# Optimization experiments

Measured on AMD Instinct MI355X. Metric: run time of the kernel, lower is better.

## Reference

```python
import jax, jax.numpy as jnp
import numpy as np

HEADS = 8
DIM_HEAD = 64
SCALE = DIM_HEAD ** -0.5


def setup_inputs() -> dict:
    key = jax.random.key(0)
    k1, k2, k3, k4 = jax.random.split(key, 4)
    b, c, f, h, w = 2, 512, 16, 32, 32
    x = jax.random.normal(k1, (b, c, f, h, w), dtype=jnp.float32)
    pos_bias = jax.random.normal(k2, (HEADS, f, f), dtype=jnp.float32)
    # torch Linear(dim, 3*hidden, bias=False): store as (in, out) for right-matmul
    w_qkv = jax.random.normal(k3, (c, 3 * HEADS * DIM_HEAD), dtype=jnp.float32) * (c ** -0.5)
    w_out = jax.random.normal(k4, (HEADS * DIM_HEAD, c), dtype=jnp.float32) * ((HEADS * DIM_HEAD) ** -0.5)
    return {"x": x, "pos_bias": pos_bias, "w_qkv": w_qkv, "w_out": w_out}


def reference(x, pos_bias, w_qkv, w_out):
    b, c, f, h, w = x.shape
    # 'b c f h w -> (b h w) f c'
    xt = jnp.transpose(x, (0, 3, 4, 2, 1)).reshape(b * h * w, f, c)
    qkv = xt @ w_qkv  # (B, f, 3*hidden)
    q, k, v = jnp.split(qkv, 3, axis=-1)
    def to_heads(t):  # (B, f, h*d) -> (B, heads, f, d)
        return t.reshape(t.shape[0], f, HEADS, DIM_HEAD).transpose(0, 2, 1, 3)
    q, k, v = to_heads(q) * SCALE, to_heads(k), to_heads(v)
    sim = jnp.einsum('bhid,bhjd->bhij', q, k)
    sim = sim + pos_bias  # (heads, f, f) broadcasts over batch
    attn = jax.nn.softmax(sim, axis=-1)  # stable max-subtract softmax
    out = jnp.einsum('bhij,bhjd->bhid', attn, v)
    out = out.transpose(0, 2, 1, 3).reshape(b * h * w, f, HEADS * DIM_HEAD)
    out = out @ w_out  # (B, f, c)
    # '(b h w) f c -> b c f h w'
    return out.reshape(b, h, w, f, c).transpose(0, 4, 3, 1, 2)
```

## Files before the change

kernel.cpp:

```cpp
#include <hip/hip_runtime.h>

typedef unsigned short u16;
typedef unsigned int u32;
typedef unsigned long long u64;
typedef __attribute__((ext_vector_type(8))) short short8;
typedef __attribute__((ext_vector_type(4))) float f32x4;

__device__ __forceinline__ u16 f2bf(float f) {
  u32 u = __builtin_bit_cast(u32, f);
  u += 0x7fffu + ((u >> 16) & 1u);
  return (u16)(u >> 16);
}
__device__ __forceinline__ u32 pk2bf(float a, float b) {
  return (u32)f2bf(a) | ((u32)f2bf(b) << 16);
}

__device__ __forceinline__ void async16(const void* g, void* l) {
  __builtin_amdgcn_global_load_lds(
      (const __attribute__((address_space(1))) u32*)g,
      (__attribute__((address_space(3))) u32*)l, 16, 0, 0);
}

__global__ __launch_bounds__(256) void k_wt(const float* __restrict__ in,
                                            u16* __restrict__ outT,
                                            int K, int N, int scaleN, int perm) {
  const int bid = blockIdx.x;
  const int ntiles = N >> 5;
  const int nt = bid % ntiles, kt = bid / ntiles;
  const int n0 = nt << 5, k0 = kt << 5;
  __shared__ float tile[32][33];
  const int t = threadIdx.x;
#pragma unroll
  for (int i = 0; i < 4; ++i) {
    const int e = t + i * 256, r = e >> 5, c = e & 31;
    tile[c][r] = in[(size_t)(k0 + r) * N + n0 + c];
  }
  __syncthreads();
#pragma unroll
  for (int i = 0; i < 4; ++i) {
    const int e = t + i * 256, r = e >> 5, c = e & 31;
    float v = tile[r][c];
    if (n0 + r < scaleN) v *= 0.125f;
    const int kcol = k0 + c;
    const int kp = perm ? ((kcol & ~63) | ((kcol & 15) << 2) | ((kcol >> 4) & 3))
                        : kcol;
    outT[(size_t)(n0 + r) * K + kp] = f2bf(v);
  }
}

__global__ __launch_bounds__(256) void k_xt(const float* __restrict__ x,
                                            u16* __restrict__ XT) {
  const int bid = blockIdx.x;
  const int plane = bid & 31;
  const int rest = bid >> 5;
  const int mt = rest & 31, ct = rest >> 5;
  const int bb = plane >> 4, f = plane & 15;
  const int m0 = mt << 5, c0 = ct << 5;
  __shared__ float tile[32][36];
  const int t = threadIdx.x;
  const int lr = t >> 3, lc = t & 7;
  const float4 v4 = *(const float4*)
      &x[((size_t)((bb * 512 + c0 + lr) * 16 + f)) * 1024 + m0 + lc * 4];
  *(float4*)&tile[lr][lc * 4] = v4;
  __syncthreads();
  const int m = t >> 3, cc = t & 7;
  union { u32 uu[2]; u64 q; } pk;
  pk.uu[0] = pk2bf(tile[cc * 4 + 0][m], tile[cc * 4 + 1][m]);
  pk.uu[1] = pk2bf(tile[cc * 4 + 2][m], tile[cc * 4 + 3][m]);
  *(u64*)&XT[((size_t)((bb * 1024 + m0 + m) * 16 + f)) * 512 + c0 + cc * 4] = pk.q;
}

struct A3St { u16 A[128][64]; u16 B[192][64]; };
struct A3At { u16 q[8][16][64]; u16 k[8][16][64]; u16 vt[8][64][16]; u16 pad[16]; };
union A3Sm { A3St st; A3At at; };

__global__ __launch_bounds__(256) void k_qkv_attn(const u16* __restrict__ XT,
                                                  const u16* __restrict__ WQ,
                                                  const float* __restrict__ pos_bias,
                                                  u16* __restrict__ AO) {
  const int tid = threadIdx.x;
  const int w = tid >> 6, lane = tid & 63;
  const int c15 = lane & 15, quad = lane >> 4;
  const int bid = blockIdx.x;
  const int hd = bid >> 8, m0 = (bid & 255) << 7;

  __shared__ A3Sm sm;

  const int lr = lane >> 3, lcb = lane & 7;

  const u16* aptr[4];
  const u16* bptr[6];
#pragma unroll
  for (int t2 = 0; t2 < 4; ++t2) {
    const int r = w * 32 + t2 * 8 + lr;
    aptr[t2] = XT + (size_t)(m0 + r) * 512 + ((lcb ^ (r & 7)) << 3);
  }
#pragma unroll
  for (int t2 = 0; t2 < 6; ++t2) {
    const int j = w * 48 + t2 * 8 + lr;
    const int grow = (j >> 6) * 512 + hd * 64 + (j & 63);
    bptr[t2] = WQ + (size_t)grow * 512 + ((lcb ^ (j & 7)) << 3);
  }

  f32x4 acc[3][8];
#pragma unroll
  for (int c = 0; c < 3; ++c)
#pragma unroll
    for (int mt = 0; mt < 8; ++mt) acc[c][mt] = f32x4{0.f, 0.f, 0.f, 0.f};

#pragma unroll
  for (int kk = 0; kk < 8; ++kk) {
    __syncthreads();
#pragma unroll
    for (int t2 = 0; t2 < 4; ++t2)
      async16(aptr[t2] + (kk << 6), &sm.st.A[w * 32 + t2 * 8][0]);
#pragma unroll
    for (int t2 = 0; t2 < 6; ++t2)
      async16(bptr[t2] + (kk << 6), &sm.st.B[w * 48 + t2 * 8][0]);
    __syncthreads();
#pragma unroll
    for (int half = 0; half < 2; ++half) {
      short8 af[8], bt[3];
#pragma unroll
      for (int mt = 0; mt < 8; ++mt) {
        const int row = mt * 16 + c15;
        const int swz = (((half << 2) + quad) ^ (row & 7)) << 3;
        af[mt] = *(const short8*)&sm.st.A[row][swz];
      }
#pragma unroll
      for (int c = 0; c < 3; ++c) {
        const int row = c * 64 + w * 16 + c15;
        const int swz = (((half << 2) + quad) ^ (row & 7)) << 3;
        bt[c] = *(const short8*)&sm.st.B[row][swz];
      }
#pragma unroll
      for (int c = 0; c < 3; ++c)
#pragma unroll
        for (int mt = 0; mt < 8; ++mt)
          acc[c][mt] = __builtin_amdgcn_mfma_f32_16x16x32_bf16(af[mt], bt[c], acc[c][mt], 0, 0, 0);
    }
  }
  __syncthreads();

  const int dloc = w * 16 + c15;
  const int ch_b = dloc >> 3, dl = dloc & 7;
#pragma unroll
  for (int mt = 0; mt < 8; ++mt) {
#pragma unroll
    for (int r = 0; r < 4; ++r) {
      const int f = quad * 4 + r;
      const int sw = ((ch_b ^ (f & 7)) << 3) | dl;
      sm.at.q[mt][f][sw] = f2bf(acc[0][mt][r]);
      sm.at.k[mt][f][sw] = f2bf(acc[1][mt][r]);
    }
    union { u32 uu[2]; u64 q; } pv;
    pv.uu[0] = pk2bf(acc[2][mt][0], acc[2][mt][1]);
    pv.uu[1] = pk2bf(acc[2][mt][2], acc[2][mt][3]);
    *(u64*)&sm.at.vt[mt][dloc][quad * 4] = pv.q;
  }
  __syncthreads();

  float pb[4];
#pragma unroll
  for (int r = 0; r < 4; ++r)
    pb[r] = pos_bias[hd * 256 + (quad * 4 + r) * 16 + c15];

  for (int sblk = 0; sblk < 2; ++sblk) {
    const int s = w * 2 + sblk;
    f32x4 sacc = f32x4{0.f, 0.f, 0.f, 0.f};
#pragma unroll
    for (int h = 0; h < 2; ++h) {
      const int chunk = (((h << 2) + quad) ^ (c15 & 7)) << 3;
      const short8 aq = *(const short8*)&sm.at.q[s][c15][chunk];
      const short8 bk = *(const short8*)&sm.at.k[s][c15][chunk];
      sacc = __builtin_amdgcn_mfma_f32_16x16x32_bf16(aq, bk, sacc, 0, 0, 0);
    }
    asm volatile("" ::: "memory");
    u16* lp = &sm.at.q[s][0][0];
#pragma unroll
    for (int e = 0; e < 4; ++e) lp[c15 * 32 + 16 + quad * 4 + e] = 0;
#pragma unroll
    for (int r = 0; r < 4; ++r) {
      float sv = sacc[r] + pb[r];
      float mx = sv;
      mx = fmaxf(mx, __shfl_xor(mx, 1));
      mx = fmaxf(mx, __shfl_xor(mx, 2));
      mx = fmaxf(mx, __shfl_xor(mx, 4));
      mx = fmaxf(mx, __shfl_xor(mx, 8));
      const float e = __expf(sv - mx);
      float sum = e;
      sum += __shfl_xor(sum, 1);
      sum += __shfl_xor(sum, 2);
      sum += __shfl_xor(sum, 4);
      sum += __shfl_xor(sum, 8);
      lp[(quad * 4 + r) * 32 + c15] = f2bf(e / sum);
    }
    asm volatile("" ::: "memory");
    const short8 ap = *(const short8*)&lp[c15 * 32 + quad * 8];
    f32x4 oacc[4];
#pragma unroll
    for (int t = 0; t < 4; ++t) {
      const short8 bv = *(const short8*)&sm.at.vt[s][t * 16 + c15][(quad & 1) * 8];
      oacc[t] = __builtin_amdgcn_mfma_f32_16x16x32_bf16(ap, bv, f32x4{0.f, 0.f, 0.f, 0.f}, 0, 0, 0);
    }
    const int s_g = (m0 >> 4) + s;
    const int bb = s_g >> 10, sp = s_g & 1023;
#pragma unroll
    for (int r = 0; r < 4; ++r) {
      union { u32 uu[2]; uint2 v; } pk;
      pk.uu[0] = pk2bf(oacc[0][r], oacc[1][r]);
      pk.uu[1] = pk2bf(oacc[2][r], oacc[3][r]);
      *(uint2*)(AO + ((size_t)(bb * 16384 + (quad * 4 + r) * 1024 + sp)) * 512 +
                hd * 64 + c15 * 4) = pk.v;
    }
  }
}

struct K2St { u16 A[128][64]; u16 B[128][64]; };
union K2Sm { K2St st; float C[64][130]; };

__global__ __launch_bounds__(256) void k_proj(const u16* __restrict__ AO,
                                              const u16* __restrict__ WO,
                                              float* __restrict__ out) {
  const int tid = threadIdx.x, w = tid >> 6, lane = tid & 63;
  const int c15 = lane & 15, quad = lane >> 4;
  const int bid = blockIdx.x;
  const int mb = bid & 255, nb = bid >> 8;
  const int m0 = mb << 7, n0 = nb << 7;
  const int b = m0 >> 14, mloc = m0 & 16383;
  __shared__ K2Sm sm;
  f32x4 acc[8][2];
#pragma unroll
  for (int mt = 0; mt < 8; ++mt) {
    acc[mt][0] = f32x4{0.f, 0.f, 0.f, 0.f};
    acc[mt][1] = f32x4{0.f, 0.f, 0.f, 0.f};
  }
  const int lr = lane >> 3, lcb = lane & 7;
  const u16* aptr[4];
  const u16* bptr[4];
#pragma unroll
  for (int t2 = 0; t2 < 4; ++t2) {
    const int r = w * 32 + t2 * 8 + lr;
    const int sw = (lcb ^ (r & 7)) << 3;
    aptr[t2] = AO + (size_t)(m0 + r) * 512 + sw;
    bptr[t2] = WO + (size_t)(n0 + r) * 512 + sw;
  }
#pragma unroll
  for (int kk = 0; kk < 8; ++kk) {
    __syncthreads();
#pragma unroll
    for (int t2 = 0; t2 < 4; ++t2) {
      async16(aptr[t2] + (kk << 6), &sm.st.A[w * 32 + t2 * 8][0]);
      async16(bptr[t2] + (kk << 6), &sm.st.B[w * 32 + t2 * 8][0]);
    }
    __syncthreads();
#pragma unroll
    for (int half = 0; half < 2; ++half) {
      short8 af[8], bt[2];
#pragma unroll
      for (int mt = 0; mt < 8; ++mt) {
        const int row = mt * 16 + c15;
        const int swz = (((half << 2) + quad) ^ (row & 7)) << 3;
        af[mt] = *(const short8*)&sm.st.A[row][swz];
      }
#pragma unroll
      for (int nt = 0; nt < 2; ++nt) {
        const int row = w * 32 + nt * 16 + c15;
        const int swz = (((half << 2) + quad) ^ (row & 7)) << 3;
        bt[nt] = *(const short8*)&sm.st.B[row][swz];
      }
#pragma unroll
      for (int mt = 0; mt < 8; ++mt) {
        acc[mt][0] = __builtin_amdgcn_mfma_f32_16x16x32_bf16(af[mt], bt[0], acc[mt][0], 0, 0, 0);
        acc[mt][1] = __builtin_amdgcn_mfma_f32_16x16x32_bf16(af[mt], bt[1], acc[mt][1], 0, 0, 0);
      }
    }
  }
  __syncthreads();
#pragma unroll
  for (int h = 0; h < 2; ++h) {
#pragma unroll
    for (int mt2 = 0; mt2 < 4; ++mt2) {
      const int mt = h * 4 + mt2;
#pragma unroll
      for (int nt = 0; nt < 2; ++nt)
#pragma unroll
        for (int r = 0; r < 4; ++r)
          sm.C[mt2 * 16 + quad * 4 + r][w * 32 + nt * 16 + c15] = acc[mt][nt][r];
    }
    __syncthreads();
    for (int jj = 0; jj < 32; ++jj) {
      const int ch = n0 + w * 32 + jj;
      out[(size_t)(b * 512 + ch) * 16384 + mloc + h * 64 + lane] = sm.C[lane][w * 32 + jj];
    }
    __syncthreads();
  }
}

extern "C" void kernel_launch(void* const* d_in, const int* in_sizes, int n_in,
                              void* d_out, int out_size, void* d_ws, size_t ws_size,
                              hipStream_t stream) {
  const float* x = (const float*)d_in[0];
  const float* pos_bias = (const float*)d_in[1];
  const float* w_qkv = (const float*)d_in[2];
  const float* w_out = (const float*)d_in[3];
  float* out = (float*)d_out;
  char* ws = (char*)d_ws;
  u16* XT = (u16*)(ws);
  u16* AO = (u16*)(ws + (size_t)33554432);
  u16* WQ = (u16*)(ws + (size_t)67108864);
  u16* WO = (u16*)(ws + (size_t)68681728);

  hipLaunchKernelGGL(k_wt, dim3(768), dim3(256), 0, stream, w_qkv, WQ, 512, 1536, 512, 0);
  hipLaunchKernelGGL(k_wt, dim3(256), dim3(256), 0, stream, w_out, WO, 512, 512, 0, 1);
  hipLaunchKernelGGL(k_xt, dim3(16384), dim3(256), 0, stream, x, XT);
  hipLaunchKernelGGL(k_qkv_attn, dim3(2048), dim3(256), 0, stream, XT, WQ, pos_bias, AO);
  hipLaunchKernelGGL(k_proj, dim3(1024), dim3(256), 0, stream, AO, WO, out);
}
```

Measured before the change: 242.4 us.

## Double-buffer K-loop LDS tiles with async prefetch in QKV and projection GEMMs

Both GEMM kernels now split each K step into 32-wide chunks held in two LDS buffers. The global-to-LDS async load of the next chunk is issued before the MFMAs on the current chunk, with one barrier per iteration instead of two. This is meant to hide global load latency behind matrix math. In exchange there are twice as many loop iterations, a narrower 4-way swizzle that may add LDS bank conflicts, and a reliance on the trailing barrier to order the async loads.

After: 244.8 us. About the same (+1.0%).

```diff
diff --git a/kernel.cpp b/kernel.cpp
--- a/kernel.cpp
+++ b/kernel.cpp
@@ -70,9 +70,9 @@
   *(u64*)&XT[((size_t)((bb * 1024 + m0 + m) * 16 + f)) * 512 + c0 + cc * 4] = pk.q;
 }
 
-struct A3St { u16 A[128][64]; u16 B[192][64]; };
+struct A3St32 { u16 A[128][32]; u16 B[192][32]; };
 struct A3At { u16 q[8][16][64]; u16 k[8][16][64]; u16 vt[8][64][16]; u16 pad[16]; };
-union A3Sm { A3St st; A3At at; };
+union A3Sm { A3St32 st[2]; A3At at; };
 
 __global__ __launch_bounds__(256) void k_qkv_attn(const u16* __restrict__ XT,
                                                   const u16* __restrict__ WQ,
@@ -86,20 +86,20 @@
 
   __shared__ A3Sm sm;
 
-  const int lr = lane >> 3, lcb = lane & 7;
-
-  const u16* aptr[4];
-  const u16* bptr[6];
-#pragma unroll
-  for (int t2 = 0; t2 < 4; ++t2) {
-    const int r = w * 32 + t2 * 8 + lr;
-    aptr[t2] = XT + (size_t)(m0 + r) * 512 + ((lcb ^ (r & 7)) << 3);
-  }
-#pragma unroll
-  for (int t2 = 0; t2 < 6; ++t2) {
-    const int j = w * 48 + t2 * 8 + lr;
+  const int lr16 = lane >> 2, lc4 = lane & 3;
+
+  const u16* aptr[2];
+  const u16* bptr[3];
+#pragma unroll
+  for (int t2 = 0; t2 < 2; ++t2) {
+    const int r = w * 32 + t2 * 16 + lr16;
+    aptr[t2] = XT + (size_t)(m0 + r) * 512 + ((lc4 ^ (r & 3)) << 3);
+  }
+#pragma unroll
+  for (int t2 = 0; t2 < 3; ++t2) {
+    const int j = w * 48 + t2 * 16 + lr16;
     const int grow = (j >> 6) * 512 + hd * 64 + (j & 63);
-    bptr[t2] = WQ + (size_t)grow * 512 + ((lcb ^ (j & 7)) << 3);
+    bptr[t2] = WQ + (size_t)grow * 512 + ((lc4 ^ (j & 3)) << 3);
   }
 
   f32x4 acc[3][8];
@@ -109,38 +109,44 @@
     for (int mt = 0; mt < 8; ++mt) acc[c][mt] = f32x4{0.f, 0.f, 0.f, 0.f};
 
 #pragma unroll
-  for (int kk = 0; kk < 8; ++kk) {
+  for (int t2 = 0; t2 < 2; ++t2)
+    async16(aptr[t2], &sm.st[0].A[w * 32 + t2 * 16][0]);
+#pragma unroll
+  for (int t2 = 0; t2 < 3; ++t2)
+    async16(bptr[t2], &sm.st[0].B[w * 48 + t2 * 16][0]);
+  __syncthreads();
+
+#pragma unroll
+  for (int kk = 0; kk < 16; ++kk) {
+    const int cur = kk & 1, nxt = cur ^ 1;
+    if (kk < 15) {
+#pragma unroll
+      for (int t2 = 0; t2 < 2; ++t2)
+        async16(aptr[t2] + ((kk + 1) << 5), &sm.st[nxt].A[w * 32 + t2 * 16][0]);
+#pragma unroll
+      for (int t2 = 0; t2 < 3; ++t2)
+        async16(bptr[t2] + ((kk + 1) << 5), &sm.st[nxt].B[w * 48 + t2 * 16][0]);
+    }
+    short8 af[8], bt[3];
+#pragma unroll
+    for (int mt = 0; mt < 8; ++mt) {
+      const int row = mt * 16 + c15;
+      const int swz = (quad ^ (row & 3)) << 3;
+      af[mt] = *(const short8*)&sm.st[cur].A[row][swz];
+    }
+#pragma unroll
+    for (int c = 0; c < 3; ++c) {
+      const int row = c * 64 + w * 16 + c15;
+      const int swz = (quad ^ (row & 3)) << 3;
+      bt[c] = *(const short8*)&sm.st[cur].B[row][swz];
+    }
+#pragma unroll
+    for (int c = 0; c < 3; ++c)
+#pragma unroll
+      for (int mt = 0; mt < 8; ++mt)
+        acc[c][mt] = __builtin_amdgcn_mfma_f32_16x16x32_bf16(af[mt], bt[c], acc[c][mt], 0, 0, 0);
     __syncthreads();
-#pragma unroll
-    for (int t2 = 0; t2 < 4; ++t2)
-      async16(aptr[t2] + (kk << 6), &sm.st.A[w * 32 + t2 * 8][0]);
-#pragma unroll
-    for (int t2 = 0; t2 < 6; ++t2)
-      async16(bptr[t2] + (kk << 6), &sm.st.B[w * 48 + t2 * 8][0]);
-    __syncthreads();
-#pragma unroll
-    for (int half = 0; half < 2; ++half) {
-      short8 af[8], bt[3];
-#pragma unroll
-      for (int mt = 0; mt < 8; ++mt) {
-        const int row = mt * 16 + c15;
-        const int swz = (((half << 2) + quad) ^ (row & 7)) << 3;
-        af[mt] = *(const short8*)&sm.st.A[row][swz];
-      }
-#pragma unroll
-      for (int c = 0; c < 3; ++c) {
-        const int row = c * 64 + w * 16 + c15;
-        const int swz = (((half << 2) + quad) ^ (row & 7)) << 3;
-        bt[c] = *(const short8*)&sm.st.B[row][swz];
-      }
-#pragma unroll
-      for (int c = 0; c < 3; ++c)
-#pragma unroll
-        for (int mt = 0; mt < 8; ++mt)
-          acc[c][mt] = __builtin_amdgcn_mfma_f32_16x16x32_bf16(af[mt], bt[c], acc[c][mt], 0, 0, 0);
-    }
-  }
-  __syncthreads();
+  }
 
   const int dloc = w * 16 + c15;
   const int ch_b = dloc >> 3, dl = dloc & 7;
@@ -216,8 +222,8 @@
   }
 }
 
-struct K2St { u16 A[128][64]; u16 B[128][64]; };
-union K2Sm { K2St st; float C[64][130]; };
+struct K2St32 { u16 A[128][32]; u16 B[128][32]; };
+union K2Sm { K2St32 st[2]; float C[64][130]; };
 
 __global__ __launch_bounds__(256) void k_proj(const u16* __restrict__ AO,
                                               const u16* __restrict__ WO,
@@ -235,48 +241,53 @@
     acc[mt][0] = f32x4{0.f, 0.f, 0.f, 0.f};
     acc[mt][1] = f32x4{0.f, 0.f, 0.f, 0.f};
   }
-  const int lr = lane >> 3, lcb = lane & 7;
-  const u16* aptr[4];
-  const u16* bptr[4];
-#pragma unroll
-  for (int t2 = 0; t2 < 4; ++t2) {
-    const int r = w * 32 + t2 * 8 + lr;
-    const int sw = (lcb ^ (r & 7)) << 3;
+  const int lr16 = lane >> 2, lc4 = lane & 3;
+  const u16* aptr[2];
+  const u16* bptr[2];
+#pragma unroll
+  for (int t2 = 0; t2 < 2; ++t2) {
+    const int r = w * 32 + t2 * 16 + lr16;
+    const int sw = (lc4 ^ (r & 3)) << 3;
     aptr[t2] = AO + (size_t)(m0 + r) * 512 + sw;
     bptr[t2] = WO + (size_t)(n0 + r) * 512 + sw;
   }
 #pragma unroll
-  for (int kk = 0; kk < 8; ++kk) {
+  for (int t2 = 0; t2 < 2; ++t2) {
+    async16(aptr[t2], &sm.st[0].A[w * 32 + t2 * 16][0]);
+    async16(bptr[t2], &sm.st[0].B[w * 32 + t2 * 16][0]);
+  }
+  __syncthreads();
+
+#pragma unroll
+  for (int kk = 0; kk < 16; ++kk) {
+    const int cur = kk & 1, nxt = cur ^ 1;
+    if (kk < 15) {
+#pragma unroll
+      for (int t2 = 0; t2 < 2; ++t2) {
+        async16(aptr[t2] + ((kk + 1) << 5), &sm.st[nxt].A[w * 32 + t2 * 16][0]);
+        async16(bptr[t2] + ((kk + 1) << 5), &sm.st[nxt].B[w * 32 + t2 * 16][0]);
+      }
+    }
+    short8 af[8], bt[2];
+#pragma unroll
+    for (int mt = 0; mt < 8; ++mt) {
+      const int row = mt * 16 + c15;
+      const int swz = (quad ^ (row & 3)) << 3;
+      af[mt] = *(const short8*)&sm.st[cur].A[row][swz];
+    }
+#pragma unroll
+    for (int nt = 0; nt < 2; ++nt) {
+      const int row = w * 32 + nt * 16 + c15;
+      const int swz = (quad ^ (row & 3)) << 3;
+      bt[nt] = *(const short8*)&sm.st[cur].B[row][swz];
+    }
+#pragma unroll
+    for (int mt = 0; mt < 8; ++mt) {
+      acc[mt][0] = __builtin_amdgcn_mfma_f32_16x16x32_bf16(af[mt], bt[0], acc[mt][0], 0, 0, 0);
+      acc[mt][1] = __builtin_amdgcn_mfma_f32_16x16x32_bf16(af[mt], bt[1], acc[mt][1], 0, 0, 0);
+    }
     __syncthreads();
-#pragma unroll
-    for (int t2 = 0; t2 < 4; ++t2) {
-      async16(aptr[t2] + (kk << 6), &sm.st.A[w * 32 + t2 * 8][0]);
-      async16(bptr[t2] + (kk << 6), &sm.st.B[w * 32 + t2 * 8][0]);
-    }
-    __syncthreads();
-#pragma unroll
-    for (int half = 0; half < 2; ++half) {
-      short8 af[8], bt[2];
-#pragma unroll
-      for (int mt = 0; mt < 8; ++mt) {
-        const int row = mt * 16 + c15;
-        const int swz = (((half << 2) + quad) ^ (row & 7)) << 3;
-        af[mt] = *(const short8*)&sm.st.A[row][swz];
-      }
-#pragma unroll
-      for (int nt = 0; nt < 2; ++nt) {
-        const int row = w * 32 + nt * 16 + c15;
-        const int swz = (((half << 2) + quad) ^ (row & 7)) << 3;
-        bt[nt] = *(const short8*)&sm.st.B[row][swz];
-      }
-#pragma unroll
-      for (int mt = 0; mt < 8; ++mt) {
-        acc[mt][0] = __builtin_amdgcn_mfma_f32_16x16x32_bf16(af[mt], bt[0], acc[mt][0], 0, 0, 0);
-        acc[mt][1] = __builtin_amdgcn_mfma_f32_16x16x32_bf16(af[mt], bt[1], acc[mt][1], 0, 0, 0);
-      }
-    }
-  }
-  __syncthreads();
+  }
 #pragma unroll
   for (int h = 0; h < 2; ++h) {
 #pragma unroll
```
